# Kernel optimization log

Measured on AMD Instinct MI355X. Metric: run time of the kernel, lower is better.

## Reference

```python
import jax, jax.numpy as jnp
import numpy as np

B = 8192         # graphs per batch
NPG = 39         # nodes per graph (from 4560 = 40*(105+9))
N = B * NPG      # total nodes
DEG = 8          # avg degree
E = N * DEG      # total edges
NEG_SLOPE = 0.2


def _glorot(key, shape):
    fan = sum(shape) if len(shape) > 1 else shape[0] + 1
    s = jnp.sqrt(6.0 / fan)
    return jax.random.uniform(key, shape, jnp.float32, -s, s)


def setup_inputs() -> dict:
    key = jax.random.key(0)
    ks = jax.random.split(key, 32)
    x = jax.random.normal(ks[0], (N, 1), jnp.float32)
    # edges constrained within each graph
    epg = NPG * DEG
    off = jnp.repeat(jnp.arange(B, dtype=jnp.int64) * NPG, epg)
    src = jax.random.randint(ks[1], (B * epg,), 0, NPG, jnp.int64) + off
    dst = jax.random.randint(ks[2], (B * epg,), 0, NPG, jnp.int64) + off
    edge_index = jnp.stack([src, dst], 0)
    batch_ids = jnp.repeat(jnp.arange(B, dtype=jnp.int64), NPG)
    dims = [(1, 8), (8, 64), (64, 32), (32, 9)]
    p = {}
    ki = 3
    for li, (fi, fo) in enumerate(dims, 1):
        p[f'W{li}'] = _glorot(ks[ki], (fi, fo)); ki += 1
        p[f'as{li}'] = _glorot(ks[ki], (fo,)); ki += 1
        p[f'ad{li}'] = _glorot(ks[ki], (fo,)); ki += 1
        p[f'b{li}'] = jnp.zeros((fo,), jnp.float32)
    p['lw1'] = _glorot(ks[ki], (4560, 1024)); ki += 1
    p['lb1'] = jnp.zeros((1024,), jnp.float32)
    p['lw2'] = _glorot(ks[ki], (1024, 128)); ki += 1
    p['lb2'] = jnp.zeros((128,), jnp.float32)
    p['lw3'] = _glorot(ks[ki], (128, 9)); ki += 1
    p['lb3'] = jnp.zeros((9,), jnp.float32)
    return {'x': x, 'edge_index': edge_index, 'batch_ids': batch_ids, **p}


def gat_layer(x, src, dst, W, a_s, a_d, b):
    # PyG GATConv, heads=1: h=xW; e_ij = LeakyReLU(a_s.h[src]+a_d.h[dst]);
    # softmax per destination node; out = sum_j alpha * h[src] + bias
    h = x @ W                                   # [N, Fo]
    s_n = h @ a_s                               # [N]
    d_n = h @ a_d                               # [N]
    e = jax.nn.leaky_relu(s_n[src] + d_n[dst], NEG_SLOPE)   # [E+N]
    m = jax.ops.segment_max(e, dst, num_segments=N)
    w = jnp.exp(e - m[dst])
    denom = jax.ops.segment_sum(w, dst, num_segments=N)
    alpha = w / (denom[dst] + 1e-16)
    out = jax.ops.segment_sum(h[src] * alpha[:, None], dst, num_segments=N)
    return out + b


def reference(x, edge_index, batch_ids, W1, as1, ad1, b1, W2, as2, ad2, b2,
              W3, as3, ad3, b3, W4, as4, ad4, b4, lw1, lb1, lw2, lb2, lw3, lb3):
    # add self-loops (PyG GATConv default)
    sl = jnp.arange(N, dtype=edge_index.dtype)
    src = jnp.concatenate([edge_index[0], sl])
    dst = jnp.concatenate([edge_index[1], sl])
    pool = lambda h: jax.ops.segment_max(h, batch_ids, num_segments=B)

    x0 = x.reshape(-1, 1)
    res = x0.reshape(B, -1)
    out0 = pool(x0)
    h1 = jax.nn.relu(gat_layer(x0, src, dst, W1, as1, ad1, b1))
    res1, out1 = h1.reshape(B, -1), pool(h1)
    h2 = jax.nn.relu(gat_layer(h1, src, dst, W2, as2, ad2, b2))
    res2, out2 = h2.reshape(B, -1), pool(h2)
    h3 = jax.nn.relu(gat_layer(h2, src, dst, W3, as3, ad3, b3))
    res3, out3 = h3.reshape(B, -1), pool(h3)
    h4 = jax.nn.relu(gat_layer(h3, src, dst, W4, as4, ad4, b4))
    res4, out4 = h4.reshape(B, -1), pool(h4)

    f = jnp.concatenate([res, res1, res2, res3, res4,
                         out0, out1, out2, out3, out4], axis=1)  # [B, 4560]
    f = jax.nn.relu(f @ lw1 + lb1)
    f = jax.nn.relu(f @ lw2 + lb2)
    return f @ lw3 + lb3
```

## Files before the change

kernel.cpp:

```cpp
#include <hip/hip_runtime.h>

#define NPG   39
#define NGRAPH 8192
#define EPG   312
#define EDG   351
#define E0    2555904
#define FDIM  4560
#define KP    4608

typedef __bf16 bf16x8 __attribute__((ext_vector_type(8)));
typedef float  f32x4  __attribute__((ext_vector_type(4)));

__device__ __forceinline__ unsigned short f2b(float f) {
  unsigned int u = __float_as_uint(f);
  u += 0x7fffu + ((u >> 16) & 1u);
  return (unsigned short)(u >> 16);
}
__device__ __forceinline__ unsigned int pk2(float lo, float hi) {
  return (unsigned int)f2b(lo) | ((unsigned int)f2b(hi) << 16);
}
__device__ __forceinline__ float b2f(unsigned short u) {
  return __uint_as_float((unsigned int)u << 16);
}
__device__ __forceinline__ void wsync() {
  asm volatile("s_waitcnt lgkmcnt(0)" ::: "memory");
}
__device__ __forceinline__ void gsync() {
  asm volatile("s_waitcnt vmcnt(0) lgkmcnt(0)" ::: "memory");
}

__shared__ alignas(16) unsigned short Htb[32 * 64];
__shared__ alignas(16) unsigned short alf16[40 * 64];
__shared__ float sn[40];
__shared__ float dn[48];
__shared__ unsigned char csr_src[EDG + 1];
__shared__ unsigned short csr_ptr[NPG + 1];

template<int Fi, int Fo, int KPAD, int KT1, int NT_STORE, int HALVES,
         int DT, int SCOL, int DCOL>
__device__ __forceinline__ void layerM(float x0,
                                       const unsigned short* __restrict__ Wb,
                                       const float* __restrict__ W1,
                                       const float* __restrict__ as1,
                                       const float* __restrict__ ad1,
                                       const float* __restrict__ bias,
                                       unsigned short* __restrict__ f_row,
                                       int in_off, int res_off, int out_off,
                                       int lane) {
  constexpr int NTH = NT_STORE / HALVES;
  constexpr int VW  = (HALVES == 2) ? 32 : Fo;
  constexpr bool SWZST = (VW == 32);
  const int r15 = lane & 15, g = lane >> 4;
  const f32x4 z = {0.f, 0.f, 0.f, 0.f};
  const uint4 z4 = {0u, 0u, 0u, 0u};
  unsigned short* stg = Htb;

#pragma unroll
  for (int i = 0; i < 5; ++i) *(uint4*)&alf16[lane * 8 + i * 512] = z4;

  if constexpr (Fi == 1) {
    float was = 0.f, wad = 0.f;
#pragma unroll
    for (int o = 0; o < 8; ++o) { float w = W1[o]; was += w * as1[o]; wad += w * ad1[o]; }
    if (lane < NPG) {
      sn[lane] = x0 * was; dn[lane] = x0 * wad;
#pragma unroll
      for (int o = 0; o < 8; ++o) {
        int idx = o * 64 + ((((lane >> 3) ^ (o & 7)) << 3)) + (lane & 7);
        Htb[idx] = f2b(x0 * W1[o]);
      }
    }
  } else {
    gsync();
    f32x4 cd[3];
#pragma unroll
    for (int mt = 0; mt < 3; ++mt) cd[mt] = z;
#pragma unroll
    for (int kt = 0; kt < KT1; ++kt) {
      bf16x8 aF[3];
#pragma unroll
      for (int mt = 0; mt < 3; ++mt) {
        int row = 16 * mt + r15;
        row = (row > 39) ? 39 : row;
        aF[mt] = *(const bf16x8*)&f_row[in_off + row * Fi + kt * 32 + g * 8];
      }
      bf16x8 bD = *(const bf16x8*)&Wb[(16 * DT + r15) * KPAD + kt * 32 + g * 8];
#pragma unroll
      for (int mt = 0; mt < 3; ++mt)
        cd[mt] = __builtin_amdgcn_mfma_f32_16x16x32_bf16(aF[mt], bD, cd[mt], 0, 0, 0);
    }
#pragma unroll
    for (int mt = 0; mt < 3; ++mt)
#pragma unroll
      for (int v = 0; v < 4; ++v) {
        float t = cd[mt][v] + __shfl_xor(cd[mt][v], 4);
        int r = 16 * mt + g * 4 + v;
        if (r15 == SCOL && r < NPG) sn[r] = t;
        if (r15 == DCOL && r < NPG) dn[r] = t;
      }
  }
  wsync();

  if (lane < NPG) {
    int rs = csr_ptr[lane], re = csr_ptr[lane + 1];
    float dv = dn[lane];
    float m = -3.4e38f;
    for (int k = rs; k < re; ++k) {
      float e = sn[csr_src[k]] + dv;
      e = (e >= 0.f) ? e : 0.2f * e;
      m = fmaxf(m, e);
    }
    float den = 0.f;
    for (int k = rs; k < re; ++k) {
      int s = csr_src[k];
      float e = sn[s] + dv;
      e = (e >= 0.f) ? e : 0.2f * e;
      float w = __expf(e - m);
      int idx = lane * 64 + ((((s >> 3) ^ (lane & 7)) << 3)) + (s & 7);
      float cur = b2f(alf16[idx]);
      unsigned short nb = f2b(cur + w);
      alf16[idx] = nb;
      den += b2f(nb) - cur;
    }
    dn[lane] = 1.f / (den + 1e-16f);
  }
  wsync();

  float invr[3][4];
#pragma unroll
  for (int mt = 0; mt < 3; ++mt)
#pragma unroll
    for (int v = 0; v < 4; ++v) invr[mt][v] = dn[16 * mt + g * 4 + v];

  float pool_[NT_STORE];
#pragma unroll
  for (int s = 0; s < NT_STORE; ++s) pool_[s] = 0.f;

#pragma unroll
  for (int h = 0; h < HALVES; ++h) {
    const int colbase = (HALVES == 2) ? 32 * h : 0;
    if constexpr (Fi > 1) {
      f32x4 c1[3][NTH];
#pragma unroll
      for (int mt = 0; mt < 3; ++mt)
#pragma unroll
        for (int tl = 0; tl < NTH; ++tl) c1[mt][tl] = z;
#pragma unroll
      for (int kt = 0; kt < KT1; ++kt) {
        bf16x8 aF[3];
#pragma unroll
        for (int mt = 0; mt < 3; ++mt) {
          int row = 16 * mt + r15;
          row = (row > 39) ? 39 : row;
          aF[mt] = *(const bf16x8*)&f_row[in_off + row * Fi + kt * 32 + g * 8];
        }
#pragma unroll
        for (int tl = 0; tl < NTH; ++tl) {
          int nt = h * NTH + tl;
          bf16x8 bW = *(const bf16x8*)&Wb[(16 * nt + r15) * KPAD + kt * 32 + g * 8];
#pragma unroll
          for (int mt = 0; mt < 3; ++mt)
            c1[mt][tl] = __builtin_amdgcn_mfma_f32_16x16x32_bf16(aF[mt], bW, c1[mt][tl], 0, 0, 0);
        }
      }
#pragma unroll
      for (int tl = 0; tl < NTH; ++tl) {
        int p = r15 + 16 * tl;
#pragma unroll
        for (int mt = 0; mt < 3; ++mt) {
          uint2 w;
          w.x = pk2(c1[mt][tl][0], c1[mt][tl][1]);
          w.y = pk2(c1[mt][tl][2], c1[mt][tl][3]);
          int idx = p * 64 + (((2 * mt + (g >> 1)) ^ (p & 7)) << 3) + (g & 1) * 4;
          *(uint2*)&Htb[idx] = w;
        }
      }
    }
    wsync();
    f32x4 c2[3][NTH];
#pragma unroll
    for (int mt = 0; mt < 3; ++mt)
#pragma unroll
      for (int tl = 0; tl < NTH; ++tl) c2[mt][tl] = z;
#pragma unroll
    for (int kt = 0; kt < 2; ++kt) {
      bf16x8 aA[3];
#pragma unroll
      for (int mt = 0; mt < 3; ++mt) {
        int row = 16 * mt + r15;
        aA[mt] = *(const bf16x8*)&alf16[row * 64 + ((((4 * kt + g) ^ (row & 7))) << 3)];
      }
#pragma unroll
      for (int tl = 0; tl < NTH; ++tl) {
        int p = r15 + 16 * tl;
        bf16x8 bH = *(const bf16x8*)&Htb[p * 64 + ((((4 * kt + g) ^ (p & 7))) << 3)];
#pragma unroll
        for (int mt = 0; mt < 3; ++mt)
          c2[mt][tl] = __builtin_amdgcn_mfma_f32_16x16x32_bf16(aA[mt], bH, c2[mt][tl], 0, 0, 0);
      }
    }
#pragma unroll
    for (int tl = 0; tl < NTH; ++tl) {
      int c = r15 + 16 * (h * NTH + tl);
      float bv = (c < Fo) ? bias[c] : 0.f;
#pragma unroll
      for (int mt = 0; mt < 3; ++mt)
#pragma unroll
        for (int v = 0; v < 4; ++v) {
          int r = 16 * mt + g * 4 + v;
          float val = fmaxf(c2[mt][tl][v] * invr[mt][v] + bv, 0.f);
          if (r < NPG && c < Fo) {
            int sc = c - colbase;
            int so = SWZST ? ((sc >> 3) ^ ((r >> 2) & 3)) : (sc >> 3);
            stg[r * VW + (so << 3) + (sc & 7)] = f2b(val);
            pool_[h * NTH + tl] = fmaxf(pool_[h * NTH + tl], val);
          }
        }
    }
    wsync();

    if constexpr (Fo == 9) {
      for (int j = lane; j < 43; j += 64)
        *(uint4*)&f_row[res_off + j * 8] = *(const uint4*)&stg[j * 8];
      if (lane < 7) f_row[res_off + 344 + lane] = stg[344 + lane];
    } else {
      constexpr int OPR = VW / 8;
      for (int j = lane; j < NPG * OPR; j += 64) {
        int r = (OPR == 4) ? (j >> 2) : j;
        int o = (OPR == 4) ? (j & 3) : 0;
        int so = SWZST ? (o ^ ((r >> 2) & 3)) : o;
        *(uint4*)&f_row[res_off + r * Fo + colbase + 8 * o] =
            *(const uint4*)&stg[r * VW + 8 * so];
      }
    }
    wsync();
  }

#pragma unroll
  for (int s = 0; s < NT_STORE; ++s) {
    float pv = pool_[s];
    pv = fmaxf(pv, __shfl_xor(pv, 16));
    pv = fmaxf(pv, __shfl_xor(pv, 32));
    int c = r15 + 16 * s;
    if (g == 0 && c < Fo) f_row[out_off + c] = f2b(pv);
  }
}

__global__ __launch_bounds__(64, 4) void gat_fused(
    const float* __restrict__ x, const int* __restrict__ ei,
    const float* __restrict__ W1, const float* __restrict__ as1, const float* __restrict__ ad1,
    const float* __restrict__ b1, const float* __restrict__ b2,
    const float* __restrict__ b3, const float* __restrict__ b4,
    const unsigned short* __restrict__ Wb,
    unsigned short* __restrict__ f) {
  const int b = blockIdx.x;
  const int lane = threadIdx.x;
  const int base = b * NPG;
  const int* srcg = ei + (size_t)b * EPG;
  const int* dstg = ei + E0 + (size_t)b * EPG;
  unsigned short* f_row = f + (size_t)b * KP;
  int* cnt = (int*)sn;
  const uint4 z4 = {0u, 0u, 0u, 0u};

#pragma unroll
  for (int i = 0; i < 4; ++i) *(uint4*)&Htb[lane * 8 + i * 512] = z4;

  float xv = 0.f;
  if (lane < NPG) {
    xv = x[(size_t)base + lane];
    f_row[lane] = f2b(xv);
  }
  if (lane == 0) f_row[39] = 0;
  if (lane < KP - 4561) f_row[4561 + lane] = 0;
  float mx = (lane < NPG) ? xv : -3.4e38f;
#pragma unroll
  for (int st = 1; st < 64; st <<= 1) { float t = __shfl_xor(mx, st); mx = fmaxf(mx, t); }
  if (lane == 0) f_row[4447] = f2b(mx);
  if (lane < NPG) cnt[lane] = 1;
  wsync();

  int es[5], ed[5];
#pragma unroll
  for (int it = 0; it < 5; ++it) {
    int e = lane + 64 * it;
    if (e < EPG) {
      int s = srcg[e] - base, d = dstg[e] - base;
      s = min(max(s, 0), NPG - 1);
      d = min(max(d, 0), NPG - 1);
      es[it] = s; ed[it] = d;
      atomicAdd(&cnt[d], 1);
    } else { es[it] = -1; ed[it] = 0; }
  }
  wsync();

  int c = (lane < NPG) ? cnt[lane] : 0;
  int v = c;
#pragma unroll
  for (int off = 1; off < 64; off <<= 1) { int t = __shfl_up(v, off); if (lane >= off) v += t; }
  int excl = v - c;
  if (lane < NPG) csr_ptr[lane] = (unsigned short)excl;
  if (lane == NPG - 1) csr_ptr[NPG] = (unsigned short)EDG;
  wsync();
  if (lane < NPG) cnt[lane] = excl;
  wsync();

  if (lane < NPG) { int p = atomicAdd(&cnt[lane], 1); csr_src[p] = (unsigned char)lane; }
#pragma unroll
  for (int it = 0; it < 5; ++it) {
    if (es[it] >= 0) {
      int p = atomicAdd(&cnt[ed[it]], 1);
      p = min(p, EDG - 1);
      csr_src[p] = (unsigned char)es[it];
    }
  }
  wsync();

  const unsigned short* Wb2 = Wb;
  const unsigned short* Wb3 = Wb + 2560;
  const unsigned short* Wb4 = Wb + 5632;

  layerM< 1,  8,  0,  0,  1,  1,  0,  0,  0>(xv, nullptr, W1, as1, ad1, b1, f_row, 0,    40,   4448, lane);
  layerM< 8, 64, 32,  1,  4,  2,  4,  0,  1>(0.f, Wb2, nullptr, nullptr, nullptr, b2, f_row, 40,   352,  4456, lane);
  layerM<64, 32, 64,  2,  2,  1,  2,  0,  1>(0.f, Wb3, nullptr, nullptr, nullptr, b3, f_row, 352,  2848, 4520, lane);
  layerM<32,  9, 32,  1,  1,  1,  0, 10, 11>(0.f, Wb4, nullptr, nullptr, nullptr, b4, f_row, 2848, 4096, 4552, lane);
}

__global__ __launch_bounds__(256) void prep_wb(
    const float* __restrict__ W2, const float* __restrict__ as2, const float* __restrict__ ad2,
    const float* __restrict__ W3, const float* __restrict__ as3, const float* __restrict__ ad3,
    const float* __restrict__ W4, const float* __restrict__ as4, const float* __restrict__ ad4,
    unsigned short* __restrict__ Wb) {
  const int tid = threadIdx.x;
  for (int i = tid; i < 80 * 32; i += 256) {
    int o = i >> 5, k = i & 31; float v = 0.f;
    if (k < 8) {
      if (o < 64) v = W2[k * 64 + o];
      else if (o == 64 || o == 68) { float s = 0; for (int j = 0; j < 64; ++j) s += W2[k * 64 + j] * as2[j];
        float hi = b2f(f2b(s)); v = (o == 64) ? hi : (s - hi); }
      else if (o == 65 || o == 69) { float s = 0; for (int j = 0; j < 64; ++j) s += W2[k * 64 + j] * ad2[j];
        float hi = b2f(f2b(s)); v = (o == 65) ? hi : (s - hi); }
    }
    Wb[i] = f2b(v);
  }
  for (int i = tid; i < 48 * 64; i += 256) {
    int o = i >> 6, k = i & 63; float v = 0.f;
    if (o < 32) v = W3[k * 32 + o];
    else if (o == 32 || o == 36) { float s = 0; for (int j = 0; j < 32; ++j) s += W3[k * 32 + j] * as3[j];
      float hi = b2f(f2b(s)); v = (o == 32) ? hi : (s - hi); }
    else if (o == 33 || o == 37) { float s = 0; for (int j = 0; j < 32; ++j) s += W3[k * 32 + j] * ad3[j];
      float hi = b2f(f2b(s)); v = (o == 33) ? hi : (s - hi); }
    Wb[2560 + i] = f2b(v);
  }
  for (int i = tid; i < 16 * 32; i += 256) {
    int o = i >> 5, k = i & 31; float v = 0.f;
    if (o < 9) v = W4[k * 9 + o];
    else if (o == 10 || o == 14) { float s = 0; for (int j = 0; j < 9; ++j) s += W4[k * 9 + j] * as4[j];
      float hi = b2f(f2b(s)); v = (o == 10) ? hi : (s - hi); }
    else if (o == 11 || o == 15) { float s = 0; for (int j = 0; j < 9; ++j) s += W4[k * 9 + j] * ad4[j];
      float hi = b2f(f2b(s)); v = (o == 11) ? hi : (s - hi); }
    Wb[5632 + i] = f2b(v);
  }
}

template<bool PERM>
__global__ __launch_bounds__(256) void tcast(const float* __restrict__ in,
                                             unsigned short* __restrict__ out,
                                             int K, int NN, int Kpad) {
  __shared__ float tile[64 * 65];
  const int k0 = blockIdx.x * 64, n0 = blockIdx.y * 64;
  const int tid = threadIdx.x;
#pragma unroll
  for (int i = 0; i < 16; ++i) {
    int idx = i * 256 + tid;
    int r = idx >> 6, c = idx & 63;
    int k = k0 + r;
    int ko;
    if constexpr (PERM) {
      ko = (k < 39) ? k : ((k == 39 || k > FDIM) ? -1 : k - 1);
    } else {
      ko = (k < K) ? k : -1;
    }
    tile[r * 65 + c] = (ko >= 0) ? in[(size_t)ko * NN + n0 + c] : 0.f;
  }
  __syncthreads();
#pragma unroll
  for (int i = 0; i < 16; ++i) {
    int idx = i * 256 + tid;
    int r = idx >> 6, c = idx & 63;
    out[(size_t)(n0 + r) * Kpad + k0 + c] = f2b(tile[c * 65 + r]);
  }
}

template<bool OUT_BF16>
__global__ __launch_bounds__(256) void mfma_gemm(const unsigned short* __restrict__ A,
    const unsigned short* __restrict__ Bt, unsigned short* __restrict__ Cb,
    float* __restrict__ Cf, const float* __restrict__ bias, int K, int N, int gridN) {
  __shared__ alignas(16) unsigned short As[2][128 * 64];
  __shared__ alignas(16) unsigned short Bs[2][128 * 64];
  const int tid = threadIdx.x;
  const int lane = tid & 63;
  const int wave = tid >> 6;
  const int wy = wave >> 1, wx = wave & 1;

  const int wg = blockIdx.x;
  const int xcd = wg & 7, idx = wg >> 3;
  const int mpr = (int)(gridDim.x >> 3) / gridN;
  const int m_local = idx / gridN;
  const int n = idx - m_local * gridN;
  const int m0 = (xcd * mpr + m_local) * 128;
  const int n0 = n * 128;

  f32x4 acc[4][4];
  const f32x4 z = {0.f, 0.f, 0.f, 0.f};
#pragma unroll
  for (int i = 0; i < 4; ++i)
#pragma unroll
    for (int j = 0; j < 4; ++j) acc[i][j] = z;

  const int srow = lane >> 3;
  const int sch  = (lane & 7) ^ srow;
  const int q    = lane >> 4;
  const int rm   = lane & 15;

#define STAGE(buf, kk0)                                                              \
  {                                                                                  \
    _Pragma("unroll")                                                                \
    for (int t = 0; t < 4; ++t) {                                                    \
      int r0 = wave * 32 + t * 8;                                                    \
      const unsigned short* ga = A  + (size_t)(m0 + r0 + srow) * K + (kk0) + sch * 8;\
      const unsigned short* gb = Bt + (size_t)(n0 + r0 + srow) * K + (kk0) + sch * 8;\
      __builtin_amdgcn_global_load_lds(                                              \
          (const __attribute__((address_space(1))) unsigned int*)(const void*)ga,    \
          (__attribute__((address_space(3))) unsigned int*)(void*)&As[buf][r0 * 64], \
          16, 0, 0);                                                                 \
      __builtin_amdgcn_global_load_lds(                                              \
          (const __attribute__((address_space(1))) unsigned int*)(const void*)gb,    \
          (__attribute__((address_space(3))) unsigned int*)(void*)&Bs[buf][r0 * 64], \
          16, 0, 0);                                                                 \
    }                                                                                \
  }

  STAGE(0, 0);
  int cur = 0;
  for (int k0 = 0; k0 < K; k0 += 64) {
    if (k0 + 64 < K) {
      STAGE(cur ^ 1, k0 + 64);
      asm volatile("s_waitcnt vmcnt(8)" ::: "memory");
    } else {
      asm volatile("s_waitcnt vmcnt(0)" ::: "memory");
    }
    __builtin_amdgcn_s_barrier();
#pragma unroll
    for (int kk = 0; kk < 2; ++kk) {
      bf16x8 af[4], bfr[4];
#pragma unroll
      for (int i = 0; i < 4; ++i) {
        int ra = wy * 64 + i * 16 + rm;
        int rb = wx * 64 + i * 16 + rm;
        af[i]  = *(const bf16x8*)&As[cur][ra * 64 + (((kk * 4 + q) ^ (ra & 7)) << 3)];
        bfr[i] = *(const bf16x8*)&Bs[cur][rb * 64 + (((kk * 4 + q) ^ (rb & 7)) << 3)];
      }
#pragma unroll
      for (int i = 0; i < 4; ++i)
#pragma unroll
        for (int j = 0; j < 4; ++j)
          acc[i][j] = __builtin_amdgcn_mfma_f32_16x16x32_bf16(af[i], bfr[j], acc[i][j], 0, 0, 0);
    }
    __builtin_amdgcn_s_barrier();
    cur ^= 1;
  }
#undef STAGE

  const int q4 = (lane >> 4) * 4;
#pragma unroll
  for (int i = 0; i < 4; ++i) {
#pragma unroll
    for (int j = 0; j < 4; ++j) {
      int row = m0 + wy * 64 + i * 16 + q4;
      int col = n0 + wx * 64 + j * 16 + rm;
      float bv = bias[col];
#pragma unroll
      for (int v = 0; v < 4; ++v) {
        float val = fmaxf(acc[i][j][v] + bv, 0.f);
        if constexpr (OUT_BF16) Cb[(size_t)(row + v) * N + col] = f2b(val);
        else                    Cf[(size_t)(row + v) * N + col] = val;
      }
    }
  }
}

__global__ __launch_bounds__(256) void mlp3(const float* __restrict__ g2,
                                            const float* __restrict__ w3,
                                            const float* __restrict__ b3,
                                            float* __restrict__ out) {
  __shared__ float gs[64 * 130];
  __shared__ float ws3[128 * 9];
  const int r0 = blockIdx.x * 64;
  const int tid = threadIdx.x;
  for (int i = tid; i < 64 * 128; i += 256)
    gs[(i >> 7) * 130 + (i & 127)] = g2[(size_t)r0 * 128 + i];
  for (int i = tid; i < 128 * 9; i += 256) ws3[i] = w3[i];
  __syncthreads();
  for (int idx = tid; idx < 64 * 9; idx += 256) {
    int r = idx / 9, c = idx - r * 9;
    float acc = b3[c];
#pragma unroll 8
    for (int k = 0; k < 128; ++k) acc += gs[r * 130 + k] * ws3[k * 9 + c];
    out[(size_t)(r0 + r) * 9 + c] = acc;
  }
}

extern "C" void kernel_launch(void* const* d_in, const int* in_sizes, int n_in,
                              void* d_out, int out_size, void* d_ws, size_t ws_size,
                              hipStream_t stream) {
  const float* x   = (const float*)d_in[0];
  const int*   ei  = (const int*)d_in[1];
  const float* W1  = (const float*)d_in[3];
  const float* as1 = (const float*)d_in[4];
  const float* ad1 = (const float*)d_in[5];
  const float* b1  = (const float*)d_in[6];
  const float* W2  = (const float*)d_in[7];
  const float* as2 = (const float*)d_in[8];
  const float* ad2 = (const float*)d_in[9];
  const float* b2  = (const float*)d_in[10];
  const float* W3  = (const float*)d_in[11];
  const float* as3 = (const float*)d_in[12];
  const float* ad3 = (const float*)d_in[13];
  const float* b3  = (const float*)d_in[14];
  const float* W4  = (const float*)d_in[15];
  const float* as4 = (const float*)d_in[16];
  const float* ad4 = (const float*)d_in[17];
  const float* b4  = (const float*)d_in[18];
  const float* lw1 = (const float*)d_in[19];
  const float* lb1 = (const float*)d_in[20];
  const float* lw2 = (const float*)d_in[21];
  const float* lb2 = (const float*)d_in[22];
  const float* lw3 = (const float*)d_in[23];
  const float* lb3 = (const float*)d_in[24];
  float* out = (float*)d_out;

  unsigned short* f   = (unsigned short*)d_ws;
  unsigned short* w1t = f   + (size_t)NGRAPH * KP;
  unsigned short* w2t = w1t + (size_t)1024 * KP;
  unsigned short* g1  = w2t + (size_t)128 * 1024;
  float*          g2  = (float*)(g1 + (size_t)NGRAPH * 1024);
  unsigned short* Wb  = g1;

  prep_wb<<<1, 256, 0, stream>>>(W2, as2, ad2, W3, as3, ad3, W4, as4, ad4, Wb);
  tcast<true ><<<dim3(KP / 64, 1024 / 64), 256, 0, stream>>>(lw1, w1t, FDIM, 1024, KP);
  tcast<false><<<dim3(1024 / 64, 128 / 64), 256, 0, stream>>>(lw2, w2t, 1024, 128, 1024);

  gat_fused<<<NGRAPH, 64, 0, stream>>>(x, ei, W1, as1, ad1,
      b1, b2, b3, b4, Wb, f);

  mfma_gemm<true ><<<512, 256, 0, stream>>>(
      f, w1t, g1, nullptr, lb1, KP, 1024, 8);
  mfma_gemm<false><<<64, 256, 0, stream>>>(
      g1, w2t, nullptr, g2, lb2, 1024, 128, 1);

  mlp3<<<NGRAPH / 64, 256, 0, stream>>>(g2, lw3, lb3, out);
}
```

Measured before the change: 211.8 us.

## Keep layer outputs in LDS and compute XW once before attention

Layer outputs of layers 1 and 3 are written to LDS (alf16) with an XOR swizzle, and the next layer reads its input from LDS instead of re-reading the global feature row. That removes the global read-after-write round trip and one gsync. The XW MFMA, previously run twice (once for the attention logits and once per half for aggregation), now runs once before the softmax and its accumulators are held in registers through the attention phase. The attention projection column reuses an existing tile when it falls inside the output tiles. In exchange register pressure rises, which could lower occupancy, and the alf16 zeroing moves after the first phase, adding one extra wavefront sync.

```diff
diff --git a/kernel.cpp b/kernel.cpp
--- a/kernel.cpp
+++ b/kernel.cpp
@@ -36,8 +36,8 @@
 __shared__ unsigned char csr_src[EDG + 1];
 __shared__ unsigned short csr_ptr[NPG + 1];
 
-template<int Fi, int Fo, int KPAD, int KT1, int NT_STORE, int HALVES,
-         int DT, int SCOL, int DCOL>
+template<int Fi, int Fo, int KPAD, int KT1, int NT, int HALVES,
+         int DT, int SCOL, int DCOL, int INSRC, int OUTDST, bool GSYNC>
 __device__ __forceinline__ void layerM(float x0,
                                        const unsigned short* __restrict__ Wb,
                                        const float* __restrict__ W1,
@@ -47,16 +47,16 @@
                                        unsigned short* __restrict__ f_row,
                                        int in_off, int res_off, int out_off,
                                        int lane) {
-  constexpr int NTH = NT_STORE / HALVES;
+  constexpr int NTH = NT / HALVES;
+  constexpr int RMASK = (Fi >= 16) ? (Fi / 8 - 1) : 0;
+  constexpr int WMASK = (Fo >= 16) ? (Fo / 8 - 1) : 0;
   constexpr int VW  = (HALVES == 2) ? 32 : Fo;
   constexpr bool SWZST = (VW == 32);
   const int r15 = lane & 15, g = lane >> 4;
   const f32x4 z = {0.f, 0.f, 0.f, 0.f};
   const uint4 z4 = {0u, 0u, 0u, 0u};
-  unsigned short* stg = Htb;
-
-#pragma unroll
-  for (int i = 0; i < 5; ++i) *(uint4*)&alf16[lane * 8 + i * 512] = z4;
+
+  f32x4 c1[3][NT];
 
   if constexpr (Fi == 1) {
     float was = 0.f, wad = 0.f;
@@ -71,34 +71,56 @@
       }
     }
   } else {
-    gsync();
+    if constexpr (GSYNC) gsync();
     f32x4 cd[3];
 #pragma unroll
     for (int mt = 0; mt < 3; ++mt) cd[mt] = z;
+#pragma unroll
+    for (int mt = 0; mt < 3; ++mt)
+#pragma unroll
+      for (int nt = 0; nt < NT; ++nt) c1[mt][nt] = z;
 #pragma unroll
     for (int kt = 0; kt < KT1; ++kt) {
       bf16x8 aF[3];
 #pragma unroll
       for (int mt = 0; mt < 3; ++mt) {
         int row = 16 * mt + r15;
-        row = (row > 39) ? 39 : row;
-        aF[mt] = *(const bf16x8*)&f_row[in_off + row * Fi + kt * 32 + g * 8];
-      }
-      bf16x8 bD = *(const bf16x8*)&Wb[(16 * DT + r15) * KPAD + kt * 32 + g * 8];
-#pragma unroll
-      for (int mt = 0; mt < 3; ++mt)
-        cd[mt] = __builtin_amdgcn_mfma_f32_16x16x32_bf16(aF[mt], bD, cd[mt], 0, 0, 0);
+        if constexpr (INSRC == 2) {
+          row = (row > 39) ? 39 : row;
+          aF[mt] = *(const bf16x8*)&f_row[in_off + row * Fi + kt * 32 + g * 8];
+        } else {
+          aF[mt] = *(const bf16x8*)&alf16[row * Fi + (((kt * 4 + g) ^ (row & RMASK)) << 3)];
+        }
+      }
+      if constexpr (DT >= NT) {
+        bf16x8 bD = *(const bf16x8*)&Wb[(16 * DT + r15) * KPAD + kt * 32 + g * 8];
+#pragma unroll
+        for (int mt = 0; mt < 3; ++mt)
+          cd[mt] = __builtin_amdgcn_mfma_f32_16x16x32_bf16(aF[mt], bD, cd[mt], 0, 0, 0);
+      }
+#pragma unroll
+      for (int nt = 0; nt < NT; ++nt) {
+        bf16x8 bW = *(const bf16x8*)&Wb[(16 * nt + r15) * KPAD + kt * 32 + g * 8];
+#pragma unroll
+        for (int mt = 0; mt < 3; ++mt)
+          c1[mt][nt] = __builtin_amdgcn_mfma_f32_16x16x32_bf16(aF[mt], bW, c1[mt][nt], 0, 0, 0);
+      }
     }
 #pragma unroll
     for (int mt = 0; mt < 3; ++mt)
 #pragma unroll
       for (int v = 0; v < 4; ++v) {
-        float t = cd[mt][v] + __shfl_xor(cd[mt][v], 4);
+        float base = (DT >= NT) ? cd[mt][v] : c1[mt][DT][v];
+        float t = base + __shfl_xor(base, 4);
         int r = 16 * mt + g * 4 + v;
         if (r15 == SCOL && r < NPG) sn[r] = t;
         if (r15 == DCOL && r < NPG) dn[r] = t;
       }
   }
+  wsync();
+
+#pragma unroll
+  for (int i = 0; i < 5; ++i) *(uint4*)&alf16[lane * 8 + i * 512] = z4;
   wsync();
 
   if (lane < NPG) {
@@ -132,45 +154,22 @@
 #pragma unroll
     for (int v = 0; v < 4; ++v) invr[mt][v] = dn[16 * mt + g * 4 + v];
 
-  float pool_[NT_STORE];
-#pragma unroll
-  for (int s = 0; s < NT_STORE; ++s) pool_[s] = 0.f;
+  float pool_[NT];
+#pragma unroll
+  for (int s = 0; s < NT; ++s) pool_[s] = 0.f;
 
 #pragma unroll
   for (int h = 0; h < HALVES; ++h) {
     const int colbase = (HALVES == 2) ? 32 * h : 0;
     if constexpr (Fi > 1) {
-      f32x4 c1[3][NTH];
-#pragma unroll
-      for (int mt = 0; mt < 3; ++mt)
-#pragma unroll
-        for (int tl = 0; tl < NTH; ++tl) c1[mt][tl] = z;
-#pragma unroll
-      for (int kt = 0; kt < KT1; ++kt) {
-        bf16x8 aF[3];
-#pragma unroll
-        for (int mt = 0; mt < 3; ++mt) {
-          int row = 16 * mt + r15;
-          row = (row > 39) ? 39 : row;
-          aF[mt] = *(const bf16x8*)&f_row[in_off + row * Fi + kt * 32 + g * 8];
-        }
-#pragma unroll
-        for (int tl = 0; tl < NTH; ++tl) {
-          int nt = h * NTH + tl;
-          bf16x8 bW = *(const bf16x8*)&Wb[(16 * nt + r15) * KPAD + kt * 32 + g * 8];
-#pragma unroll
-          for (int mt = 0; mt < 3; ++mt)
-            c1[mt][tl] = __builtin_amdgcn_mfma_f32_16x16x32_bf16(aF[mt], bW, c1[mt][tl], 0, 0, 0);
-        }
-      }
 #pragma unroll
       for (int tl = 0; tl < NTH; ++tl) {
         int p = r15 + 16 * tl;
 #pragma unroll
         for (int mt = 0; mt < 3; ++mt) {
           uint2 w;
-          w.x = pk2(c1[mt][tl][0], c1[mt][tl][1]);
-          w.y = pk2(c1[mt][tl][2], c1[mt][tl][3]);
+          w.x = pk2(c1[mt][h * NTH + tl][0], c1[mt][h * NTH + tl][1]);
+          w.y = pk2(c1[mt][h * NTH + tl][2], c1[mt][h * NTH + tl][3]);
           int idx = p * 64 + (((2 * mt + (g >> 1)) ^ (p & 7)) << 3) + (g & 1) * 4;
           *(uint2*)&Htb[idx] = w;
         }
@@ -210,34 +209,47 @@
           int r = 16 * mt + g * 4 + v;
           float val = fmaxf(c2[mt][tl][v] * invr[mt][v] + bv, 0.f);
           if (r < NPG && c < Fo) {
-            int sc = c - colbase;
-            int so = SWZST ? ((sc >> 3) ^ ((r >> 2) & 3)) : (sc >> 3);
-            stg[r * VW + (so << 3) + (sc & 7)] = f2b(val);
+            if constexpr (OUTDST == 1) {
+              alf16[r * Fo + ((((c >> 3) ^ (r & WMASK)) << 3) | (c & 7))] = f2b(val);
+            } else {
+              int sc = c - colbase;
+              int so = SWZST ? ((sc >> 3) ^ ((r >> 2) & 3)) : (sc >> 3);
+              Htb[r * VW + (so << 3) + (sc & 7)] = f2b(val);
+            }
             pool_[h * NTH + tl] = fmaxf(pool_[h * NTH + tl], val);
           }
         }
     }
     wsync();
 
-    if constexpr (Fo == 9) {
+    if constexpr (OUTDST == 1) {
+      if constexpr (Fo == 8) {
+        if (lane < NPG)
+          *(uint4*)&f_row[res_off + lane * 8] = *(const uint4*)&alf16[lane * 8];
+      } else {
+        for (int j = lane; j < NPG * 4; j += 64) {
+          int r = j >> 2, o = j & 3;
+          *(uint4*)&f_row[res_off + r * 32 + 8 * o] =
+              *(const uint4*)&alf16[r * 32 + ((o ^ (r & 3)) << 3)];
+        }
+      }
+    } else if constexpr (Fo == 9) {
       for (int j = lane; j < 43; j += 64)
-        *(uint4*)&f_row[res_off + j * 8] = *(const uint4*)&stg[j * 8];
-      if (lane < 7) f_row[res_off + 344 + lane] = stg[344 + lane];
+        *(uint4*)&f_row[res_off + j * 8] = *(const uint4*)&Htb[j * 8];
+      if (lane < 7) f_row[res_off + 344 + lane] = Htb[344 + lane];
     } else {
-      constexpr int OPR = VW / 8;
-      for (int j = lane; j < NPG * OPR; j += 64) {
-        int r = (OPR == 4) ? (j >> 2) : j;
-        int o = (OPR == 4) ? (j & 3) : 0;
-        int so = SWZST ? (o ^ ((r >> 2) & 3)) : o;
+      for (int j = lane; j < NPG * 4; j += 64) {
+        int r = j >> 2, o = j & 3;
+        int so = o ^ ((r >> 2) & 3);
         *(uint4*)&f_row[res_off + r * Fo + colbase + 8 * o] =
-            *(const uint4*)&stg[r * VW + 8 * so];
+            *(const uint4*)&Htb[r * VW + 8 * so];
       }
     }
     wsync();
   }
 
 #pragma unroll
-  for (int s = 0; s < NT_STORE; ++s) {
+  for (int s = 0; s < NT; ++s) {
     float pv = pool_[s];
     pv = fmaxf(pv, __shfl_xor(pv, 16));
     pv = fmaxf(pv, __shfl_xor(pv, 32));
@@ -319,10 +331,10 @@
   const unsigned short* Wb3 = Wb + 2560;
   const unsigned short* Wb4 = Wb + 5632;
 
-  layerM< 1,  8,  0,  0,  1,  1,  0,  0,  0>(xv, nullptr, W1, as1, ad1, b1, f_row, 0,    40,   4448, lane);
-  layerM< 8, 64, 32,  1,  4,  2,  4,  0,  1>(0.f, Wb2, nullptr, nullptr, nullptr, b2, f_row, 40,   352,  4456, lane);
-  layerM<64, 32, 64,  2,  2,  1,  2,  0,  1>(0.f, Wb3, nullptr, nullptr, nullptr, b3, f_row, 352,  2848, 4520, lane);
-  layerM<32,  9, 32,  1,  1,  1,  0, 10, 11>(0.f, Wb4, nullptr, nullptr, nullptr, b4, f_row, 2848, 4096, 4552, lane);
+  layerM< 1,  8,  0,  0,  1,  1,  0,  0,  0,   0,    1,  false>(xv, nullptr, W1, as1, ad1, b1, f_row, 0,    40,   4448, lane);
+  layerM< 8, 64, 32,  1,  4,  2,  4,  0,  1,   1,    0,  false>(0.f, Wb2, nullptr, nullptr, nullptr, b2, f_row, 0,    352,  4456, lane);
+  layerM<64, 32, 64,  2,  2,  1,  2,  0,  1,   2,    1,  true >(0.f, Wb3, nullptr, nullptr, nullptr, b3, f_row, 352,  2848, 4520, lane);
+  layerM<32,  9, 32,  1,  1,  1,  0, 10, 11,   1,    0,  false>(0.f, Wb4, nullptr, nullptr, nullptr, b4, f_row, 0,    4096, 4552, lane);
 }
 
 __global__ __launch_bounds__(256) void prep_wb(
```

After: 210.7 us. Within noise of the previous version (-0.5%).
